# Kernel optimization log

Measured on AMD Instinct MI355X. Metric: run time of the kernel, lower is better.

## Reference

```python
import jax, jax.numpy as jnp
import numpy as np

B, S, HID = 1, 2048, 2048
NH = 32
NOPE, ROPE = 128, 64
QK = NOPE + ROPE
VD = 128
KV_RANK = 512
SW = 128            # sliding window (layer_types[layer_idx] == 'sliding_attention')
SCALE = QK ** -0.5
NEG = -1e9


def rotate_half(x):
    h = x.shape[-1] // 2
    return jnp.concatenate([-x[..., h:], x[..., :h]], axis=-1)


def setup_inputs() -> dict:
    key = jax.random.key(0)
    ks = jax.random.split(key, 8)

    def n(k, shape, s=0.02):
        return jax.random.normal(k, shape, dtype=jnp.float32) * s

    hidden = jax.random.normal(ks[0], (B, S, HID), dtype=jnp.float32)
    # HF-style RoPE tables, broadcast to [B, S, ROPE]
    pos = jnp.arange(S, dtype=jnp.float32)
    inv = 1.0 / (10000.0 ** (jnp.arange(0, ROPE, 2, dtype=jnp.float32) / ROPE))
    ang = pos[:, None] * inv[None, :]
    ang = jnp.concatenate([ang, ang], axis=-1)
    cos = jnp.broadcast_to(jnp.cos(ang)[None], (B, S, ROPE))
    sin = jnp.broadcast_to(jnp.sin(ang)[None], (B, S, ROPE))
    return dict(
        hidden_states=hidden, cos=cos, sin=sin,
        Wq=n(ks[1], (HID, NH * QK)), bq=jnp.zeros((NH * QK,), jnp.float32),
        Wkva=n(ks[2], (HID, KV_RANK + ROPE)), bkva=jnp.zeros((KV_RANK + ROPE,), jnp.float32),
        Wkvb=n(ks[3], (KV_RANK, NH * (NOPE + VD))),
        Wo=n(ks[4], (NH * VD, HID)), bo=jnp.zeros((HID,), jnp.float32),
        sinks=jax.random.normal(ks[5], (NH,), dtype=jnp.float32),
    )


def reference(hidden_states, cos, sin, Wq, bq, Wkva, bkva, Wkvb, Wo, bo, sinks):
    b, s = hidden_states.shape[:2]
    # Q projection -> [b, nh, s, qk_head_dim]
    q = (hidden_states @ Wq + bq).reshape(b, s, NH, QK).transpose(0, 2, 1, 3)
    q_nope, q_rope = q[..., :NOPE], q[..., NOPE:]
    # MLA: compressed KV latent + shared (MQA) rope key
    ckv = hidden_states @ Wkva + bkva                       # [b, s, rank+rope]
    kv_lat, k_rope = ckv[..., :KV_RANK], ckv[..., KV_RANK:]
    kv = (kv_lat @ Wkvb).reshape(b, s, NH, NOPE + VD).transpose(0, 2, 1, 3)
    k_nope, v = kv[..., :NOPE], kv[..., NOPE:]              # [b, nh, s, *]
    k_rope = k_rope.reshape(b, 1, s, ROPE)                  # mla_rope_num_kv_heads = 1
    # RoPE (HF apply_rotary_pos_emb, unsqueeze head dim)
    c, si = cos[:, None], sin[:, None]
    q_rope = q_rope * c + rotate_half(q_rope) * si
    k_rope = k_rope * c + rotate_half(k_rope) * si
    k_rope = jnp.broadcast_to(k_rope, (b, NH, s, ROPE))     # repeat_kv
    qs = jnp.concatenate([q_nope, q_rope], axis=-1)
    kk = jnp.concatenate([k_nope, k_rope], axis=-1)
    # attention logits with causal + sliding-window mask
    logits = jnp.einsum('bhqd,bhkd->bhqk', qs, kk) * SCALE
    i = jnp.arange(s)[:, None]
    j = jnp.arange(s)[None, :]
    allowed = (j <= i) & (i - j < SW)
    logits = jnp.where(allowed[None, None], logits, NEG)
    # sink-augmented softmax: append learned per-head sink logit, softmax, drop it
    sink = jnp.broadcast_to(sinks[None, :, None, None], (b, NH, s, 1))
    probs = jax.nn.softmax(jnp.concatenate([logits, sink], axis=-1), axis=-1)[..., :-1]
    out = jnp.einsum('bhqk,bhkd->bhqd', probs, v)           # [b, nh, s, vd]
    out = out.transpose(0, 2, 1, 3).reshape(b, s, NH * VD)
    return out @ Wo + bo
```

## Files before the change

kernel.cpp:

```cpp
#include <hip/hip_runtime.h>
#include <hip/hip_bf16.h>
#include <math.h>

#define S_LEN 2048
#define HID_DIM 2048
#define NH 32
#define NOPE 128
#define ROPE_D 64
#define QKD 192
#define VD 128
#define KV_RANK 512
#define SW 128
#define NQK (NH*QKD)
#define CKV_N (KV_RANK+ROPE_D)
#define KVN (NH*(NOPE+VD))
#define KNW (NH*NOPE)
#define OUT_HID 2048
#define ATT_SCALE 0.07216878364870323f
#define NEG_INF (-1e30f)

typedef __bf16 bf16x8 __attribute__((ext_vector_type(8)));
typedef float  f32x4  __attribute__((ext_vector_type(4)));

__device__ __forceinline__ void async_load16(const void* gp, void* lp) {
    __builtin_amdgcn_global_load_lds(
        (const __attribute__((address_space(1))) void*)gp,
        (__attribute__((address_space(3))) void*)lp, 16, 0, 0);
}

__global__ __launch_bounds__(256)
void prep(const float* __restrict__ hidden, __hip_bfloat16* __restrict__ hid_bf,
          const float* __restrict__ Wq,   __hip_bfloat16* __restrict__ WqT,
          const float* __restrict__ Wkva, __hip_bfloat16* __restrict__ WkvaT,
          const float* __restrict__ Wkvb, __hip_bfloat16* __restrict__ WkvbT,
          const float* __restrict__ Wo,   __hip_bfloat16* __restrict__ WoT)
{
    __shared__ float tile[64][65];
    int b = blockIdx.x;
    const int t = threadIdx.x;

    if (b < 4096) {
        int i = b * 256 + t;
        float4 v = ((const float4*)hidden)[i];
        hid_bf[i * 4 + 0] = __float2bfloat16(v.x);
        hid_bf[i * 4 + 1] = __float2bfloat16(v.y);
        hid_bf[i * 4 + 2] = __float2bfloat16(v.z);
        hid_bf[i * 4 + 3] = __float2bfloat16(v.w);
        return;
    }
    b -= 4096;
    const float* src; __hip_bfloat16* dst; int rows, cols, CX;
    if (b < 3072)                { src = Wq;   dst = WqT;   rows = 2048; cols = 6144; CX = 96;  }
    else if ((b -= 3072) < 288)  { src = Wkva; dst = WkvaT; rows = 2048; cols = 576;  CX = 9;   }
    else if ((b -= 288) < 1024)  { src = Wkvb; dst = WkvbT; rows = 512;  cols = 8192; CX = 128; }
    else { b -= 1024;              src = Wo;   dst = WoT;   rows = 4096; cols = 2048; CX = 32;  }

    const int bx = b % CX, by = b / CX;
    const int r0 = by * 64, c0 = bx * 64;
    const int tx = t & 63, ty = t >> 6;
    #pragma unroll
    for (int i = 0; i < 16; ++i) {
        const int rr = ty + i * 4;
        tile[rr][tx] = src[(size_t)(r0 + rr) * cols + c0 + tx];
    }
    __syncthreads();
    #pragma unroll
    for (int i = 0; i < 16; ++i) {
        const int dr = ty + i * 4;
        dst[(size_t)(c0 + dr) * rows + r0 + tx] = __float2bfloat16(tile[tx][dr]);
    }
}

#define BAR()   __builtin_amdgcn_s_barrier()
#define LGKM0() asm volatile("s_waitcnt lgkmcnt(0)" ::: "memory")
#define VMC(n)  asm volatile("s_waitcnt vmcnt(" #n ")" ::: "memory")

__device__ __forceinline__ void gemm256_core(
    const __hip_bfloat16* __restrict__ A, int lda,
    const __hip_bfloat16* __restrict__ Bt, int ldbt,
    int m0, int n0, int kbeg, int nit,
    __hip_bfloat16* lds, f32x4 (&acc)[8][4])
{
    const int t = threadIdx.x;
    const int w = t >> 6, L = t & 63;
    const int lane15 = L & 15, quad = L >> 4;
    const int wr = w >> 2, wc = w & 3;

    const int prw = w * 8 + (L >> 3);
    const int c8  = ((L & 7) ^ ((L >> 3) & 7)) * 8;
    const __hip_bfloat16* gA = A  + (size_t)(m0 + prw) * lda  + kbeg + c8;
    const __hip_bfloat16* gB = Bt + (size_t)(n0 + prw) * ldbt + kbeg + c8;
    const int uA = w * 512;
    const int uB = 16384 + w * 512;

    const int cx0 = ((quad)     ^ (L & 7)) * 8;
    const int cx1 = ((4 + quad) ^ (L & 7)) * 8;
    const int ra  = wr * 8192 + lane15 * 64;
    const int rb  = 16384 + (wc >> 1) * 8192 + (wc & 1) * 4096 + lane15 * 64;

    bf16x8 af[4][2], bfr[4][2];

    auto STG_A = [&](int buf, int h, int kt) {
        const __hip_bfloat16* g = gA + (size_t)h * 128 * lda + kt * 64;
        __hip_bfloat16* lp = lds + buf * 32768 + h * 8192 + uA;
        async_load16(g, lp);
        async_load16(g + (size_t)64 * lda, lp + 4096);
    };
    auto STG_B = [&](int buf, int h, int kt) {
        const __hip_bfloat16* g = gB + (size_t)h * 128 * ldbt + kt * 64;
        __hip_bfloat16* lp = lds + buf * 32768 + h * 8192 + uB;
        async_load16(g, lp);
        async_load16(g + (size_t)64 * ldbt, lp + 4096);
    };
    auto LDA4 = [&](int buf, int mlo) {
        const __hip_bfloat16* p0 = lds + buf * 32768 + ra;
        #pragma unroll
        for (int j = 0; j < 4; ++j) {
            af[j][0] = *(const bf16x8*)(const void*)(p0 + (mlo + j) * 1024 + cx0);
            af[j][1] = *(const bf16x8*)(const void*)(p0 + (mlo + j) * 1024 + cx1);
        }
    };
    auto LDB2 = [&](int buf, int nlo) {
        const __hip_bfloat16* p0 = lds + buf * 32768 + rb;
        #pragma unroll
        for (int n = 0; n < 2; ++n) {
            bfr[nlo + n][0] = *(const bf16x8*)(const void*)(p0 + (nlo + n) * 1024 + cx0);
            bfr[nlo + n][1] = *(const bf16x8*)(const void*)(p0 + (nlo + n) * 1024 + cx1);
        }
    };
    auto MMQ = [&](int mlo, int nlo) {
        __builtin_amdgcn_s_setprio(1);
        #pragma unroll
        for (int j = 0; j < 4; ++j)
            #pragma unroll
            for (int n = 0; n < 2; ++n)
                #pragma unroll
                for (int ks = 0; ks < 2; ++ks)
                    acc[mlo + j][nlo + n] = __builtin_amdgcn_mfma_f32_16x16x32_bf16(
                        af[j][ks], bfr[nlo + n][ks], acc[mlo + j][nlo + n], 0, 0, 0);
        __builtin_amdgcn_s_setprio(0);
    };

    STG_A(0, 0, 0); STG_B(0, 0, 0); STG_B(0, 1, 0); STG_A(0, 1, 0);
    STG_A(1, 0, 1); STG_B(1, 0, 1); STG_B(1, 1, 1);
    VMC(6);
    BAR();

    for (int it = 0; it < nit; ++it) {
        const int t0 = 2 * it, t1 = t0 + 1;
        const bool nl = (it + 1 < nit);
        LDA4(0, 0); LDB2(0, 0); STG_A(1, 1, t1);
        BAR(); LGKM0(); MMQ(0, 0); BAR();
        LDB2(0, 2);
        BAR(); LGKM0(); MMQ(0, 2); BAR();
        LDA4(0, 4); if (nl) STG_B(0, 0, t0 + 2);
        BAR(); LGKM0(); MMQ(4, 2); BAR();
        if (nl) { STG_B(0, 1, t0 + 2); STG_A(0, 0, t0 + 2); VMC(6); }
        else    { VMC(0); }
        BAR(); MMQ(4, 0); BAR();
        LDA4(1, 0); LDB2(1, 0); if (nl) STG_A(0, 1, t0 + 2);
        BAR(); LGKM0(); MMQ(0, 0); BAR();
        LDB2(1, 2);
        BAR(); LGKM0(); MMQ(0, 2); BAR();
        LDA4(1, 4); if (nl) STG_B(1, 0, t1 + 2);
        BAR(); LGKM0(); MMQ(4, 2); BAR();
        if (nl) { STG_B(1, 1, t1 + 2); STG_A(1, 0, t1 + 2); VMC(6); }
        BAR(); MMQ(4, 0); BAR();
    }
}

__global__ __launch_bounds__(512)
void gemm_q256(const __hip_bfloat16* __restrict__ A,
               const __hip_bfloat16* __restrict__ Bt,
               const float* __restrict__ bias,
               const float* __restrict__ cosb, const float* __restrict__ sinb,
               __hip_bfloat16* __restrict__ C)
{
    __shared__ __hip_bfloat16 lds[65536];
    const int m0 = blockIdx.y * 256, n0 = blockIdx.x * 256;
    f32x4 acc[8][4];
    #pragma unroll
    for (int mi = 0; mi < 8; ++mi)
        #pragma unroll
        for (int ni = 0; ni < 4; ++ni) acc[mi][ni] = (f32x4){0.f, 0.f, 0.f, 0.f};

    gemm256_core(A, HID_DIM, Bt, HID_DIM, m0, n0, 0, HID_DIM / 128, lds, acc);

    const int t = threadIdx.x;
    const int w = t >> 6, L = t & 63;
    const int lane15 = L & 15, quad = L >> 4;
    const int wr = w >> 2, wc = w & 3;
    const int ns = n0 + wc * 64;
    const bool do_rope = ((ns % 192) == 128);

    float bv[4];
    #pragma unroll
    for (int ni = 0; ni < 4; ++ni) bv[ni] = bias[ns + ni * 16 + lane15];

    #pragma unroll
    for (int mi = 0; mi < 8; ++mi) {
        const int rbase = m0 + wr * 128 + mi * 16 + quad * 4;
        float vv[4][4];
        #pragma unroll
        for (int ni = 0; ni < 4; ++ni)
            #pragma unroll
            for (int p = 0; p < 4; ++p) vv[ni][p] = acc[mi][ni][p] + bv[ni];
        if (do_rope) {
            #pragma unroll
            for (int ni = 0; ni < 2; ++ni) {
                const int dd = ni * 16 + lane15;
                #pragma unroll
                for (int p = 0; p < 4; ++p) {
                    const int srow = rbase + p;
                    const float c0 = cosb[srow * ROPE_D + dd];
                    const float c1 = cosb[srow * ROPE_D + dd + 32];
                    const float s0 = sinb[srow * ROPE_D + dd];
                    const float s1 = sinb[srow * ROPE_D + dd + 32];
                    const float x0 = vv[ni][p], x1 = vv[ni + 2][p];
                    vv[ni][p]     = x0 * c0 - x1 * s0;
                    vv[ni + 2][p] = x1 * c1 + x0 * s1;
                }
            }
        }
        #pragma unroll
        for (int ni = 0; ni < 4; ++ni) {
            const int c = ns + ni * 16 + lane15;
            #pragma unroll
            for (int p = 0; p < 4; ++p)
                C[(size_t)(rbase + p) * NQK + c] = __float2bfloat16(vv[ni][p] * ATT_SCALE);
        }
    }
}

__global__ __launch_bounds__(512)
void gemm_kv256(const __hip_bfloat16* __restrict__ A,
                const __hip_bfloat16* __restrict__ Bt,
                __hip_bfloat16* __restrict__ kn,
                __hip_bfloat16* __restrict__ vt)
{
    __shared__ __hip_bfloat16 lds[65536];
    const int m0 = blockIdx.y * 256, n0 = blockIdx.x * 256;
    f32x4 acc[8][4];
    #pragma unroll
    for (int mi = 0; mi < 8; ++mi)
        #pragma unroll
        for (int ni = 0; ni < 4; ++ni) acc[mi][ni] = (f32x4){0.f, 0.f, 0.f, 0.f};

    gemm256_core(A, KV_RANK, Bt, KV_RANK, m0, n0, 0, KV_RANK / 128, lds, acc);

    const int t = threadIdx.x;
    const int w = t >> 6, L = t & 63;
    const int lane15 = L & 15, quad = L >> 4;
    const int wr = w >> 2, wc = w & 3;
    const int ns = n0 + wc * 64;

    #pragma unroll
    for (int mi = 0; mi < 8; ++mi) {
        const int rbase = m0 + wr * 128 + mi * 16 + quad * 4;
        #pragma unroll
        for (int ni = 0; ni < 4; ++ni) {
            const int c = ns + ni * 16 + lane15;
            const int h = c >> 8, d = c & 255;
            if (d < NOPE) {
                #pragma unroll
                for (int p = 0; p < 4; ++p)
                    kn[(size_t)(rbase + p) * KNW + h * NOPE + d] = __float2bfloat16(acc[mi][ni][p]);
            } else {
                ushort4 pk;
                __hip_bfloat16 b0 = __float2bfloat16(acc[mi][ni][0]);
                __hip_bfloat16 b1 = __float2bfloat16(acc[mi][ni][1]);
                __hip_bfloat16 b2 = __float2bfloat16(acc[mi][ni][2]);
                __hip_bfloat16 b3 = __float2bfloat16(acc[mi][ni][3]);
                pk.x = *(unsigned short*)&b0; pk.y = *(unsigned short*)&b1;
                pk.z = *(unsigned short*)&b2; pk.w = *(unsigned short*)&b3;
                *(ushort4*)(vt + (size_t)(h * VD + (d - NOPE)) * S_LEN + rbase) = pk;
            }
        }
    }
}

__global__ __launch_bounds__(512)
void gemm_partial256(const __hip_bfloat16* __restrict__ A, int lda,
                     const __hip_bfloat16* __restrict__ Bt, int ldbt,
                     float* __restrict__ P, int ldp, size_t zstride, int KL)
{
    __shared__ __hip_bfloat16 lds[65536];
    const int m0 = blockIdx.y * 256, n0 = blockIdx.x * 256;
    const int z  = blockIdx.z;
    f32x4 acc[8][4];
    #pragma unroll
    for (int mi = 0; mi < 8; ++mi)
        #pragma unroll
        for (int ni = 0; ni < 4; ++ni) acc[mi][ni] = (f32x4){0.f, 0.f, 0.f, 0.f};

    gemm256_core(A, lda, Bt, ldbt, m0, n0, z * KL, KL / 128, lds, acc);

    const int t = threadIdx.x;
    const int w = t >> 6, L = t & 63;
    const int lane15 = L & 15, quad = L >> 4;
    const int wr = w >> 2, wc = w & 3;
    float* Pz = P + (size_t)z * zstride;

    #pragma unroll
    for (int mi = 0; mi < 8; ++mi) {
        const int rbase = m0 + wr * 128 + mi * 16 + quad * 4;
        #pragma unroll
        for (int ni = 0; ni < 4; ++ni) {
            const int c = n0 + wc * 64 + ni * 16 + lane15;
            #pragma unroll
            for (int p = 0; p < 4; ++p)
                Pz[(size_t)(rbase + p) * ldp + c] = acc[mi][ni][p];
        }
    }
}

__global__ __launch_bounds__(256)
void gemm_partial(const __hip_bfloat16* __restrict__ A, int lda,
                  const __hip_bfloat16* __restrict__ Bt, int ldbt,
                  float* __restrict__ P, int ldp, size_t zstride, int KL)
{
    __shared__ __hip_bfloat16 As[128 * 32];
    __shared__ __hip_bfloat16 Bs[128 * 32];

    const int t = threadIdx.x;
    const int w = t >> 6;
    const int L = t & 63;
    const int lane15 = L & 15, quad = L >> 4;
    const int wm = (w & 1) * 64, wn = (w >> 1) * 64;
    const int m0 = blockIdx.y * 128;
    const int n0 = blockIdx.x * 128;
    const int z  = blockIdx.z;
    float* Pz = P + (size_t)z * zstride;

    f32x4 acc[4][4];
    #pragma unroll
    for (int mi = 0; mi < 4; ++mi)
        #pragma unroll
        for (int ni = 0; ni < 4; ++ni)
            acc[mi][ni] = (f32x4){0.f, 0.f, 0.f, 0.f};

    const int kend = (z + 1) * KL;
    for (int k0 = z * KL; k0 < kend; k0 += 32) {
        __syncthreads();
        #pragma unroll
        for (int i = 0; i < 2; ++i) {
            const int slot = w * 64 + i * 256 + L;
            const int base = (w * 64 + i * 256) * 8;
            async_load16(A  + (size_t)(m0 + (slot >> 2)) * lda  + k0 + (slot & 3) * 8,
                         (void*)(As + base));
            async_load16(Bt + (size_t)(n0 + (slot >> 2)) * ldbt + k0 + (slot & 3) * 8,
                         (void*)(Bs + base));
        }
        __syncthreads();

        bf16x8 af[4], bfr[4];
        #pragma unroll
        for (int mi = 0; mi < 4; ++mi)
            af[mi] = *(const bf16x8*)(const void*)(As + (wm + mi * 16 + lane15) * 32 + quad * 8);
        #pragma unroll
        for (int ni = 0; ni < 4; ++ni)
            bfr[ni] = *(const bf16x8*)(const void*)(Bs + (wn + ni * 16 + lane15) * 32 + quad * 8);
        #pragma unroll
        for (int mi = 0; mi < 4; ++mi)
            #pragma unroll
            for (int ni = 0; ni < 4; ++ni)
                acc[mi][ni] = __builtin_amdgcn_mfma_f32_16x16x32_bf16(af[mi], bfr[ni], acc[mi][ni], 0, 0, 0);
    }

    #pragma unroll
    for (int mi = 0; mi < 4; ++mi) {
        const int rbase = m0 + wm + mi * 16 + quad * 4;
        #pragma unroll
        for (int ni = 0; ni < 4; ++ni) {
            const int c = n0 + wn + ni * 16 + lane15;
            #pragma unroll
            for (int p = 0; p < 4; ++p)
                Pz[(size_t)(rbase + p) * ldp + c] = acc[mi][ni][p];
        }
    }
}

__global__ __launch_bounds__(256)
void ckv_reduce(const float* __restrict__ P, const float* __restrict__ bkva,
                __hip_bfloat16* __restrict__ kvlat, __hip_bfloat16* __restrict__ kr,
                const float* __restrict__ cosb, const float* __restrict__ sinb)
{
    const int s = blockIdx.x;
    const int t = threadIdx.x;
    const size_t zs = (size_t)S_LEN * 640;
    const float* row = P + (size_t)s * 640;

    for (int c = t; c < KV_RANK; c += 256) {
        float v = row[c] + row[zs + c] + row[2 * zs + c] + row[3 * zs + c] + bkva[c];
        kvlat[(size_t)s * KV_RANK + c] = __float2bfloat16(v);
    }
    if (t < 32) {
        const int d = t;
        float a = row[512 + d] + row[zs + 512 + d] + row[2 * zs + 512 + d] + row[3 * zs + 512 + d] + bkva[512 + d];
        float b = row[544 + d] + row[zs + 544 + d] + row[2 * zs + 544 + d] + row[3 * zs + 544 + d] + bkva[544 + d];
        const float c0 = cosb[s * ROPE_D + d],      c1 = cosb[s * ROPE_D + d + 32];
        const float s0 = sinb[s * ROPE_D + d],      s1 = sinb[s * ROPE_D + d + 32];
        kr[(size_t)s * ROPE_D + d]      = __float2bfloat16(a * c0 - b * s0);
        kr[(size_t)s * ROPE_D + d + 32] = __float2bfloat16(b * c1 + a * s1);
    }
}

__global__ __launch_bounds__(256)
void wo_reduce4(const float* __restrict__ P, const float* __restrict__ bo,
                float* __restrict__ out)
{
    const size_t i = (size_t)blockIdx.x * 256 + threadIdx.x;
    const size_t zs = (size_t)S_LEN * OUT_HID;
    float4 a = ((const float4*)P)[i];
    float4 b = ((const float4*)(P + zs))[i];
    float4 c = ((const float4*)(P + 2 * zs))[i];
    float4 d = ((const float4*)(P + 3 * zs))[i];
    const int col = (int)((i * 4) & (OUT_HID - 1));
    float4 bb = *(const float4*)(bo + col);
    float4 o;
    o.x = a.x + b.x + c.x + d.x + bb.x;
    o.y = a.y + b.y + c.y + d.y + bb.y;
    o.z = a.z + b.z + c.z + d.z + bb.z;
    o.w = a.w + b.w + c.w + d.w + bb.w;
    ((float4*)out)[i] = o;
}

#define SS 170
#define SP 168
#define KSTR 200
#define VSTR 40

__global__ __launch_bounds__(256)
void attn_mfma2(const __hip_bfloat16* __restrict__ q,
                const __hip_bfloat16* __restrict__ kn,
                const __hip_bfloat16* __restrict__ kr,
                const __hip_bfloat16* __restrict__ vt,
                const float* __restrict__ sinks,
                __hip_bfloat16* __restrict__ out)
{
    __shared__ float lds_s[32 * SS];
    __shared__ __hip_bfloat16 lds_p[32 * SP];
    __shared__ __hip_bfloat16 lds_kv[32 * KSTR];

    const int h  = blockIdx.y;
    const int q0 = blockIdx.x * 32;
    const int t  = threadIdx.x;
    const int w  = t >> 6;
    const int L  = t & 63;
    const int lane15 = L & 15, quad = L >> 4;
    const int wm = (w & 1) * 16;
    const int wn = (w >> 1) * 16;

    int lo = q0 - SW + 1; if (lo < 0) lo = 0;
    const int cb = lo & ~31;
    const int nc = ((q0 - cb) >> 5) + 1;

    bf16x8 qf[6];
    {
        const __hip_bfloat16* qrow = q + (size_t)(q0 + wm + lane15) * NQK + h * QKD;
        #pragma unroll
        for (int kk = 0; kk < 6; ++kk)
            qf[kk] = *(const bf16x8*)(const void*)(qrow + kk * 32 + quad * 8);
    }

    for (int cc = 0; cc < nc; ++cc) {
        const int c0 = cb + cc * 32;
        __syncthreads();
        #pragma unroll
        for (int e = t; e < 768; e += 256) {
            const int row = e / 24, slot = e % 24;
            const int j = c0 + row;
            const __hip_bfloat16* g = (slot < 16)
                ? kn + (size_t)j * KNW + h * NOPE + slot * 8
                : kr + (size_t)j * ROPE_D + (slot - 16) * 8;
            *(bf16x8*)(void*)(lds_kv + row * KSTR + slot * 8) = *(const bf16x8*)(const void*)g;
        }
        __syncthreads();

        f32x4 s = (f32x4){0.f, 0.f, 0.f, 0.f};
        #pragma unroll
        for (int kk = 0; kk < 6; ++kk) {
            bf16x8 bf = *(const bf16x8*)(const void*)(lds_kv + (wn + lane15) * KSTR + kk * 32 + quad * 8);
            s = __builtin_amdgcn_mfma_f32_16x16x32_bf16(qf[kk], bf, s, 0, 0, 0);
        }
        const int j = c0 + wn + lane15;
        #pragma unroll
        for (int p = 0; p < 4; ++p) {
            const int i = q0 + wm + quad * 4 + p;
            const bool ok = (j <= i) && (i - j < SW);
            lds_s[(wm + quad * 4 + p) * SS + cc * 32 + wn + lane15] = ok ? s[p] : NEG_INF;
        }
    }
    __syncthreads();

    {
        const int r = t >> 3, g = t & 7;
        const int ncols = nc * 32;
        const float sink = sinks[h];
        float mx = sink;
        for (int c = g; c < ncols; c += 8)
            mx = fmaxf(mx, lds_s[r * SS + c]);
        #pragma unroll
        for (int off = 1; off < 8; off <<= 1)
            mx = fmaxf(mx, __shfl_xor(mx, off));
        float sum = 0.f;
        for (int c = g; c < ncols; c += 8) {
            float e = __expf(lds_s[r * SS + c] - mx);
            lds_s[r * SS + c] = e;
            sum += e;
        }
        #pragma unroll
        for (int off = 1; off < 8; off <<= 1)
            sum += __shfl_xor(sum, off);
        const float inv = 1.0f / (sum + __expf(sink - mx));
        for (int c = g; c < ncols; c += 8)
            lds_p[r * SP + c] = __float2bfloat16(lds_s[r * SS + c] * inv);
    }

    f32x4 oacc[4];
    #pragma unroll
    for (int ni = 0; ni < 4; ++ni) oacc[ni] = (f32x4){0.f, 0.f, 0.f, 0.f};

    for (int cc = 0; cc < nc; ++cc) {
        const int c0 = cb + cc * 32;
        __syncthreads();
        #pragma unroll
        for (int e = t; e < 512; e += 256) {
            const int row = e >> 2, slot = e & 3;
            *(bf16x8*)(void*)(lds_kv + row * VSTR + slot * 8) =
                *(const bf16x8*)(const void*)(vt + (size_t)(h * VD + row) * S_LEN + c0 + slot * 8);
        }
        __syncthreads();

        bf16x8 ap = *(const bf16x8*)(const void*)(lds_p + (wm + lane15) * SP + cc * 32 + quad * 8);
        #pragma unroll
        for (int ni = 0; ni < 4; ++ni) {
            bf16x8 bv = *(const bf16x8*)(const void*)(lds_kv + ((w >> 1) * 64 + ni * 16 + lane15) * VSTR + quad * 8);
            oacc[ni] = __builtin_amdgcn_mfma_f32_16x16x32_bf16(ap, bv, oacc[ni], 0, 0, 0);
        }
    }

    #pragma unroll
    for (int ni = 0; ni < 4; ++ni) {
        const int col = h * VD + (w >> 1) * 64 + ni * 16 + lane15;
        #pragma unroll
        for (int p = 0; p < 4; ++p) {
            const int row = q0 + wm + quad * 4 + p;
            out[(size_t)row * (NH * VD) + col] = __float2bfloat16(oacc[ni][p]);
        }
    }
}

extern "C" void kernel_launch(void* const* d_in, const int* in_sizes, int n_in,
                              void* d_out, int out_size, void* d_ws, size_t ws_size,
                              hipStream_t stream) {
    const float* hidden = (const float*)d_in[0];
    const float* cosb   = (const float*)d_in[1];
    const float* sinb   = (const float*)d_in[2];
    const float* Wq     = (const float*)d_in[3];
    const float* bq     = (const float*)d_in[4];
    const float* Wkva   = (const float*)d_in[5];
    const float* bkva   = (const float*)d_in[6];
    const float* Wkvb   = (const float*)d_in[7];
    const float* Wo     = (const float*)d_in[8];
    const float* bo     = (const float*)d_in[9];
    const float* sinks  = (const float*)d_in[10];
    float* out = (float*)d_out;

    uint8_t* p = (uint8_t*)d_ws;
    __hip_bfloat16* attn_bf = (__hip_bfloat16*)p; p += (size_t)S_LEN * NH * VD * 2;
    __hip_bfloat16* WoT     = (__hip_bfloat16*)p; p += (size_t)OUT_HID * (NH*VD) * 2;
    __hip_bfloat16* q_bf    = (__hip_bfloat16*)p; p += (size_t)S_LEN * NQK * 2;
    __hip_bfloat16* hid_bf  = (__hip_bfloat16*)p; p += (size_t)S_LEN * HID_DIM * 2;
    __hip_bfloat16* WqT     = (__hip_bfloat16*)p; p += (size_t)NQK * HID_DIM * 2;
    __hip_bfloat16* WkvaT   = (__hip_bfloat16*)p; p += (size_t)640 * HID_DIM * 2;
    __hip_bfloat16* WkvbT   = (__hip_bfloat16*)p; p += (size_t)KVN * KV_RANK * 2;
    __hip_bfloat16* kn_bf   = (__hip_bfloat16*)p; p += (size_t)S_LEN * KNW * 2;
    __hip_bfloat16* vt_bf   = (__hip_bfloat16*)p; p += (size_t)S_LEN * NH * VD * 2;
    __hip_bfloat16* kr_bf   = (__hip_bfloat16*)p; p += (size_t)S_LEN * ROPE_D * 2;
    __hip_bfloat16* kvlat   = (__hip_bfloat16*)p; p += (size_t)S_LEN * KV_RANK * 2;
    float* ckvP = (float*)WqT;
    float* WoP  = (float*)q_bf;

    prep<<<10528, 256, 0, stream>>>(hidden, hid_bf, Wq, WqT, Wkva, WkvaT,
                                    Wkvb, WkvbT, Wo, WoT);

    gemm_q256<<<dim3(NQK / 256, S_LEN / 256), 512, 0, stream>>>(
        hid_bf, WqT, bq, cosb, sinb, q_bf);

    gemm_partial<<<dim3(5, S_LEN / 128, 4), 256, 0, stream>>>(
        hid_bf, HID_DIM, WkvaT, HID_DIM, ckvP, 640, (size_t)S_LEN * 640, 512);

    ckv_reduce<<<S_LEN, 256, 0, stream>>>(ckvP, bkva, kvlat, kr_bf, cosb, sinb);

    gemm_kv256<<<dim3(KVN / 256, S_LEN / 256), 512, 0, stream>>>(
        kvlat, WkvbT, kn_bf, vt_bf);

    attn_mfma2<<<dim3(S_LEN / 32, NH), 256, 0, stream>>>(
        q_bf, kn_bf, kr_bf, vt_bf, sinks, attn_bf);

    gemm_partial256<<<dim3(OUT_HID / 256, S_LEN / 256, 4), 512, 0, stream>>>(
        attn_bf, NH * VD, WoT, NH * VD, WoP, OUT_HID, (size_t)S_LEN * OUT_HID, 1024);

    wo_reduce4<<<(S_LEN * OUT_HID / 4) / 256, 256, 0, stream>>>(WoP, bo, out);
}
```

Baseline: 379.6 us.

## Fuse Q and compressed-KV projections into one GEMM launch with fused epilogues

The Q projection and the KV-latent/rope-key projection now run in a single kernel launch. Blocks 0-191 compute Q tiles and blocks 192-215 compute 256x256 CKV tiles with the full K range. This replaces the split-K partial GEMM and its separate reduce kernel, so the fp32 partial buffers are no longer written and read back and two launches go away. Bias and RoPE for the latent and rope key move into the GEMM epilogue. In exchange, the CKV tiles are padded from 640 to 768 columns, reading weight rows past the WkvaT buffer (into the adjacent workspace) and doing some wasted MMA work on them.

```diff
diff --git a/kernel.cpp b/kernel.cpp
--- a/kernel.cpp
+++ b/kernel.cpp
@@ -170,64 +170,111 @@
 }
 
 __global__ __launch_bounds__(512)
-void gemm_q256(const __hip_bfloat16* __restrict__ A,
-               const __hip_bfloat16* __restrict__ Bt,
-               const float* __restrict__ bias,
-               const float* __restrict__ cosb, const float* __restrict__ sinb,
-               __hip_bfloat16* __restrict__ C)
+void gemm_q_ckv(const __hip_bfloat16* __restrict__ A,
+                const __hip_bfloat16* __restrict__ BtQ,
+                const __hip_bfloat16* __restrict__ BtKVA,
+                const float* __restrict__ bq,
+                const float* __restrict__ bkva,
+                const float* __restrict__ cosb, const float* __restrict__ sinb,
+                __hip_bfloat16* __restrict__ C,
+                __hip_bfloat16* __restrict__ kvlat,
+                __hip_bfloat16* __restrict__ kr)
 {
     __shared__ __hip_bfloat16 lds[65536];
-    const int m0 = blockIdx.y * 256, n0 = blockIdx.x * 256;
+    const int bid = blockIdx.x;
+    const bool is_q = (bid < 192);
+    const int m0 = (is_q ? (bid / 24) : ((bid - 192) / 3)) * 256;
+    const int n0 = (is_q ? (bid % 24) : ((bid - 192) % 3)) * 256;
+
     f32x4 acc[8][4];
     #pragma unroll
     for (int mi = 0; mi < 8; ++mi)
         #pragma unroll
         for (int ni = 0; ni < 4; ++ni) acc[mi][ni] = (f32x4){0.f, 0.f, 0.f, 0.f};
 
-    gemm256_core(A, HID_DIM, Bt, HID_DIM, m0, n0, 0, HID_DIM / 128, lds, acc);
+    gemm256_core(A, HID_DIM, is_q ? BtQ : BtKVA, HID_DIM, m0, n0, 0,
+                 HID_DIM / 128, lds, acc);
 
     const int t = threadIdx.x;
     const int w = t >> 6, L = t & 63;
     const int lane15 = L & 15, quad = L >> 4;
     const int wr = w >> 2, wc = w & 3;
     const int ns = n0 + wc * 64;
-    const bool do_rope = ((ns % 192) == 128);
-
-    float bv[4];
-    #pragma unroll
-    for (int ni = 0; ni < 4; ++ni) bv[ni] = bias[ns + ni * 16 + lane15];
-
-    #pragma unroll
-    for (int mi = 0; mi < 8; ++mi) {
-        const int rbase = m0 + wr * 128 + mi * 16 + quad * 4;
-        float vv[4][4];
-        #pragma unroll
-        for (int ni = 0; ni < 4; ++ni)
+
+    if (is_q) {
+        const bool do_rope = ((ns % 192) == 128);
+        float bv[4];
+        #pragma unroll
+        for (int ni = 0; ni < 4; ++ni) bv[ni] = bq[ns + ni * 16 + lane15];
+
+        #pragma unroll
+        for (int mi = 0; mi < 8; ++mi) {
+            const int rbase = m0 + wr * 128 + mi * 16 + quad * 4;
+            float vv[4][4];
             #pragma unroll
-            for (int p = 0; p < 4; ++p) vv[ni][p] = acc[mi][ni][p] + bv[ni];
-        if (do_rope) {
+            for (int ni = 0; ni < 4; ++ni)
+                #pragma unroll
+                for (int p = 0; p < 4; ++p) vv[ni][p] = acc[mi][ni][p] + bv[ni];
+            if (do_rope) {
+                #pragma unroll
+                for (int ni = 0; ni < 2; ++ni) {
+                    const int dd = ni * 16 + lane15;
+                    #pragma unroll
+                    for (int p = 0; p < 4; ++p) {
+                        const int srow = rbase + p;
+                        const float c0 = cosb[srow * ROPE_D + dd];
+                        const float c1 = cosb[srow * ROPE_D + dd + 32];
+                        const float s0 = sinb[srow * ROPE_D + dd];
+                        const float s1 = sinb[srow * ROPE_D + dd + 32];
+                        const float x0 = vv[ni][p], x1 = vv[ni + 2][p];
+                        vv[ni][p]     = x0 * c0 - x1 * s0;
+                        vv[ni + 2][p] = x1 * c1 + x0 * s1;
+                    }
+                }
+            }
+            #pragma unroll
+            for (int ni = 0; ni < 4; ++ni) {
+                const int c = ns + ni * 16 + lane15;
+                #pragma unroll
+                for (int p = 0; p < 4; ++p)
+                    C[(size_t)(rbase + p) * NQK + c] = __float2bfloat16(vv[ni][p] * ATT_SCALE);
+            }
+        }
+    } else if (ns < KV_RANK) {
+        float bv[4];
+        #pragma unroll
+        for (int ni = 0; ni < 4; ++ni) bv[ni] = bkva[ns + ni * 16 + lane15];
+        #pragma unroll
+        for (int mi = 0; mi < 8; ++mi) {
+            const int s = m0 + wr * 128 + mi * 16 + quad * 4;
+            #pragma unroll
+            for (int ni = 0; ni < 4; ++ni) {
+                const int c = ns + ni * 16 + lane15;
+                #pragma unroll
+                for (int p = 0; p < 4; ++p)
+                    kvlat[(size_t)(s + p) * KV_RANK + c] =
+                        __float2bfloat16(acc[mi][ni][p] + bv[ni]);
+            }
+        }
+    } else if (ns == KV_RANK) {
+        #pragma unroll
+        for (int mi = 0; mi < 8; ++mi) {
+            const int sb = m0 + wr * 128 + mi * 16 + quad * 4;
             #pragma unroll
             for (int ni = 0; ni < 2; ++ni) {
-                const int dd = ni * 16 + lane15;
+                const int d = ni * 16 + lane15;
+                const float ba = bkva[512 + d], bb = bkva[544 + d];
                 #pragma unroll
                 for (int p = 0; p < 4; ++p) {
-                    const int srow = rbase + p;
-                    const float c0 = cosb[srow * ROPE_D + dd];
-                    const float c1 = cosb[srow * ROPE_D + dd + 32];
-                    const float s0 = sinb[srow * ROPE_D + dd];
-                    const float s1 = sinb[srow * ROPE_D + dd + 32];
-                    const float x0 = vv[ni][p], x1 = vv[ni + 2][p];
-                    vv[ni][p]     = x0 * c0 - x1 * s0;
-                    vv[ni + 2][p] = x1 * c1 + x0 * s1;
+                    const int s = sb + p;
+                    const float a = acc[mi][ni][p] + ba;
+                    const float b = acc[mi][ni + 2][p] + bb;
+                    const float c0 = cosb[s * ROPE_D + d], c1 = cosb[s * ROPE_D + d + 32];
+                    const float s0 = sinb[s * ROPE_D + d], s1 = sinb[s * ROPE_D + d + 32];
+                    kr[(size_t)s * ROPE_D + d]      = __float2bfloat16(a * c0 - b * s0);
+                    kr[(size_t)s * ROPE_D + d + 32] = __float2bfloat16(b * c1 + a * s1);
                 }
             }
-        }
-        #pragma unroll
-        for (int ni = 0; ni < 4; ++ni) {
-            const int c = ns + ni * 16 + lane15;
-            #pragma unroll
-            for (int p = 0; p < 4; ++p)
-                C[(size_t)(rbase + p) * NQK + c] = __float2bfloat16(vv[ni][p] * ATT_SCALE);
         }
     }
 }
@@ -311,97 +358,6 @@
             for (int p = 0; p < 4; ++p)
                 Pz[(size_t)(rbase + p) * ldp + c] = acc[mi][ni][p];
         }
-    }
-}
-
-__global__ __launch_bounds__(256)
-void gemm_partial(const __hip_bfloat16* __restrict__ A, int lda,
-                  const __hip_bfloat16* __restrict__ Bt, int ldbt,
-                  float* __restrict__ P, int ldp, size_t zstride, int KL)
-{
-    __shared__ __hip_bfloat16 As[128 * 32];
-    __shared__ __hip_bfloat16 Bs[128 * 32];
-
-    const int t = threadIdx.x;
-    const int w = t >> 6;
-    const int L = t & 63;
-    const int lane15 = L & 15, quad = L >> 4;
-    const int wm = (w & 1) * 64, wn = (w >> 1) * 64;
-    const int m0 = blockIdx.y * 128;
-    const int n0 = blockIdx.x * 128;
-    const int z  = blockIdx.z;
-    float* Pz = P + (size_t)z * zstride;
-
-    f32x4 acc[4][4];
-    #pragma unroll
-    for (int mi = 0; mi < 4; ++mi)
-        #pragma unroll
-        for (int ni = 0; ni < 4; ++ni)
-            acc[mi][ni] = (f32x4){0.f, 0.f, 0.f, 0.f};
-
-    const int kend = (z + 1) * KL;
-    for (int k0 = z * KL; k0 < kend; k0 += 32) {
-        __syncthreads();
-        #pragma unroll
-        for (int i = 0; i < 2; ++i) {
-            const int slot = w * 64 + i * 256 + L;
-            const int base = (w * 64 + i * 256) * 8;
-            async_load16(A  + (size_t)(m0 + (slot >> 2)) * lda  + k0 + (slot & 3) * 8,
-                         (void*)(As + base));
-            async_load16(Bt + (size_t)(n0 + (slot >> 2)) * ldbt + k0 + (slot & 3) * 8,
-                         (void*)(Bs + base));
-        }
-        __syncthreads();
-
-        bf16x8 af[4], bfr[4];
-        #pragma unroll
-        for (int mi = 0; mi < 4; ++mi)
-            af[mi] = *(const bf16x8*)(const void*)(As + (wm + mi * 16 + lane15) * 32 + quad * 8);
-        #pragma unroll
-        for (int ni = 0; ni < 4; ++ni)
-            bfr[ni] = *(const bf16x8*)(const void*)(Bs + (wn + ni * 16 + lane15) * 32 + quad * 8);
-        #pragma unroll
-        for (int mi = 0; mi < 4; ++mi)
-            #pragma unroll
-            for (int ni = 0; ni < 4; ++ni)
-                acc[mi][ni] = __builtin_amdgcn_mfma_f32_16x16x32_bf16(af[mi], bfr[ni], acc[mi][ni], 0, 0, 0);
-    }
-
-    #pragma unroll
-    for (int mi = 0; mi < 4; ++mi) {
-        const int rbase = m0 + wm + mi * 16 + quad * 4;
-        #pragma unroll
-        for (int ni = 0; ni < 4; ++ni) {
-            const int c = n0 + wn + ni * 16 + lane15;
-            #pragma unroll
-            for (int p = 0; p < 4; ++p)
-                Pz[(size_t)(rbase + p) * ldp + c] = acc[mi][ni][p];
-        }
-    }
-}
-
-__global__ __launch_bounds__(256)
-void ckv_reduce(const float* __restrict__ P, const float* __restrict__ bkva,
-                __hip_bfloat16* __restrict__ kvlat, __hip_bfloat16* __restrict__ kr,
-                const float* __restrict__ cosb, const float* __restrict__ sinb)
-{
-    const int s = blockIdx.x;
-    const int t = threadIdx.x;
-    const size_t zs = (size_t)S_LEN * 640;
-    const float* row = P + (size_t)s * 640;
-
-    for (int c = t; c < KV_RANK; c += 256) {
-        float v = row[c] + row[zs + c] + row[2 * zs + c] + row[3 * zs + c] + bkva[c];
-        kvlat[(size_t)s * KV_RANK + c] = __float2bfloat16(v);
-    }
-    if (t < 32) {
-        const int d = t;
-        float a = row[512 + d] + row[zs + 512 + d] + row[2 * zs + 512 + d] + row[3 * zs + 512 + d] + bkva[512 + d];
-        float b = row[544 + d] + row[zs + 544 + d] + row[2 * zs + 544 + d] + row[3 * zs + 544 + d] + bkva[544 + d];
-        const float c0 = cosb[s * ROPE_D + d],      c1 = cosb[s * ROPE_D + d + 32];
-        const float s0 = sinb[s * ROPE_D + d],      s1 = sinb[s * ROPE_D + d + 32];
-        kr[(size_t)s * ROPE_D + d]      = __float2bfloat16(a * c0 - b * s0);
-        kr[(size_t)s * ROPE_D + d + 32] = __float2bfloat16(b * c1 + a * s1);
     }
 }
 
@@ -579,19 +535,13 @@
     __hip_bfloat16* vt_bf   = (__hip_bfloat16*)p; p += (size_t)S_LEN * NH * VD * 2;
     __hip_bfloat16* kr_bf   = (__hip_bfloat16*)p; p += (size_t)S_LEN * ROPE_D * 2;
     __hip_bfloat16* kvlat   = (__hip_bfloat16*)p; p += (size_t)S_LEN * KV_RANK * 2;
-    float* ckvP = (float*)WqT;
-    float* WoP  = (float*)q_bf;
+    float* WoP = (float*)q_bf;
 
     prep<<<10528, 256, 0, stream>>>(hidden, hid_bf, Wq, WqT, Wkva, WkvaT,
                                     Wkvb, WkvbT, Wo, WoT);
 
-    gemm_q256<<<dim3(NQK / 256, S_LEN / 256), 512, 0, stream>>>(
-        hid_bf, WqT, bq, cosb, sinb, q_bf);
-
-    gemm_partial<<<dim3(5, S_LEN / 128, 4), 256, 0, stream>>>(
-        hid_bf, HID_DIM, WkvaT, HID_DIM, ckvP, 640, (size_t)S_LEN * 640, 512);
-
-    ckv_reduce<<<S_LEN, 256, 0, stream>>>(ckvP, bkva, kvlat, kr_bf, cosb, sinb);
+    gemm_q_ckv<<<216, 512, 0, stream>>>(
+        hid_bf, WqT, WkvaT, bq, bkva, cosb, sinb, q_bf, kvlat, kr_bf);
 
     gemm_kv256<<<dim3(KVN / 256, S_LEN / 256), 512, 0, stream>>>(
         kvlat, WkvbT, kn_bf, vt_bf);
```

After: 352.4 us. 1.08x faster.
